# Kernel optimization log

Measured on AMD Instinct MI355X. Metric: run time of the kernel, lower is better.

Reference implementation:

```python
import jax, jax.numpy as jnp
import numpy as np
from jax import lax

B, T, S, D = 16, 16, 196, 768
H = 256          # hidden_dim
NH = 4           # attention heads
TH = 32          # temporal hidden = max(16, H//8)
UP = 4           # UPSAMPLE_FACTOR


def _ln(x, w, b):
    m = jnp.mean(x, -1, keepdims=True)
    v = jnp.mean((x - m) ** 2, -1, keepdims=True)
    return (x - m) / jnp.sqrt(v + 1e-5) * w + b


def _gelu(x):
    return jax.nn.gelu(x, approximate=False)  # torch nn.GELU default (erf)


def _upmat(g, f):
    # torch F.interpolate bilinear, align_corners=False, as a [g*f, g] matrix
    g_up = g * f
    src = np.maximum((np.arange(g_up) + 0.5) / f - 0.5, 0.0)
    i0 = np.minimum(np.floor(src).astype(np.int64), g - 1)
    i1 = np.minimum(i0 + 1, g - 1)
    w1 = (src - i0).astype(np.float32)
    w0 = 1.0 - w1
    W = np.zeros((g_up, g), dtype=np.float32)
    np.add.at(W, (np.arange(g_up), i0), w0)
    np.add.at(W, (np.arange(g_up), i1), w1)
    return jnp.asarray(W)


def setup_inputs() -> dict:
    key = jax.random.key(0)
    ks = jax.random.split(key, 12)
    r = lambda i, shape: jax.random.normal(ks[i], shape, jnp.float32) * 0.02
    return dict(
        tokens=jax.random.normal(ks[0], (B, T * S, D), jnp.float32),
        num_frames=T,
        fixed_box_wh=jax.random.uniform(ks[1], (2,), jnp.float32, 0.1, 0.5),
        ln_w=jnp.ones((D,), jnp.float32), ln_b=jnp.zeros((D,), jnp.float32),
        query=r(2, (1, 1, D)),
        in_proj_w=r(3, (3 * D, D)), in_proj_b=jnp.zeros((3 * D,), jnp.float32),
        out_w=r(4, (D, D)), out_b=jnp.zeros((D,), jnp.float32),
        an_w=jnp.ones((D,), jnp.float32), an_b=jnp.zeros((D,), jnp.float32),
        obj_w=r(5, (1, D)), obj_b=jnp.zeros((1,), jnp.float32),
        temperature=jnp.asarray(8.0, jnp.float32),
        r1_w=r(6, (H, 2 * D)), r1_b=jnp.zeros((H,), jnp.float32),
        r2_w=r(7, (H // 2, H)), r2_b=jnp.zeros((H // 2,), jnp.float32),
        r3_w=r(8, (2, H // 2)), r3_b=jnp.zeros((2,), jnp.float32),
        tc1_w=r(9, (TH, 2, 5)), tc1_b=jnp.zeros((TH,), jnp.float32),
        tc2_w=r(10, (2, TH, 5)), tc2_b=jnp.zeros((2,), jnp.float32),
    )


def reference(tokens, num_frames, fixed_box_wh, ln_w, ln_b, query,
              in_proj_w, in_proj_b, out_w, out_b, an_w, an_b, obj_w, obj_b,
              temperature, r1_w, r1_b, r2_w, r2_b, r3_w, r3_b,
              tc1_w, tc1_b, tc2_w, tc2_b):
    Bb, N, Dd = tokens.shape
    Tt = int(num_frames)
    Ss = N // Tt
    g = int(round(Ss ** 0.5))
    g_up = g * UP
    BT = Bb * Tt
    dt = tokens.dtype

    normed = _ln(tokens, ln_w, ln_b)
    flat = normed.reshape(BT, Ss, Dd)  # per-frame tokens

    # --- attention pooling with learned query (dropout off, eval) ---
    Wq, Wk, Wv = jnp.split(in_proj_w, 3, 0)
    bq, bk, bv = jnp.split(in_proj_b, 3, 0)
    dh = Dd // NH
    qh = (query.reshape(1, Dd) @ Wq.T + bq).reshape(NH, dh)  # same query for all frames
    kh = (flat @ Wk.T + bk).reshape(BT, Ss, NH, dh)
    vh = (flat @ Wv.T + bv).reshape(BT, Ss, NH, dh)
    scores = jnp.einsum('hd,bshd->bhs', qh, kh) / jnp.sqrt(jnp.asarray(dh, dt))
    attnp = jax.nn.softmax(scores, -1)
    ctx = jnp.einsum('bhs,bshd->bhd', attnp, vh).reshape(BT, Dd)
    pooled = _ln(ctx @ out_w.T + out_b, an_w, an_b)

    obj = (flat @ obj_w.T + obj_b)[..., 0]  # [BT,S]
    Wu = _upmat(g, UP)
    up = jnp.einsum('ug,bgh,vh->buv', Wu, obj.reshape(BT, g, g), Wu)
    up = up.reshape(BT, g_up * g_up)
    temp = jnp.maximum(temperature, 1.0)
    probs = jax.nn.softmax(up * temp, -1)
    coords = (jnp.arange(g_up, dtype=dt) + 0.5) / g_up
    yy, xx = jnp.meshgrid(coords, coords, indexing='ij')
    cx0 = probs @ xx.reshape(-1)
    cy0 = probs @ yy.reshape(-1)

    # --- 3x3 local token gather around coarse center ---
    cxg = jnp.clip(cx0 * g, 0, g - 1).astype(jnp.int32)
    cyg = jnp.clip(cy0 * g, 0, g - 1).astype(jnp.int32)
    off = jnp.array([-1, 0, 1], jnp.int32)
    gy = jnp.clip(cyg[:, None, None] + off[None, :, None], 0, g - 1)
    gx = jnp.clip(cxg[:, None, None] + off[None, None, :], 0, g - 1)
    idx = (gy * g + gx).reshape(BT, 9)
    local = jnp.take_along_axis(flat, idx[:, :, None], axis=1).mean(1)

    # --- refine MLP ---
    h1 = _gelu(jnp.concatenate([pooled, local], -1) @ r1_w.T + r1_b)
    h2 = _gelu(h1 @ r2_w.T + r2_b)
    delta = h2 @ r3_w.T + r3_b
    cx = jnp.clip(cx0 + 0.3 * jnp.tanh(delta[:, 0]), 0.0, 1.0)
    cy = jnp.clip(cy0 + 0.3 * jnp.tanh(delta[:, 1]), 0.0, 1.0)

    # --- temporal residual refiner over center trajectories ---
    seq = jnp.stack([cx, cy], 1).reshape(Bb, Tt, 2).transpose(0, 2, 1)  # [B,2,T]
    dn = ('NCH', 'OIH', 'NCH')
    t1 = _gelu(lax.conv_general_dilated(seq, tc1_w, (1,), [(2, 2)],
                                        dimension_numbers=dn) + tc1_b[None, :, None])
    td = lax.conv_general_dilated(t1, tc2_w, (1,), [(2, 2)],
                                  dimension_numbers=dn) + tc2_b[None, :, None]
    td = td.transpose(0, 2, 1).reshape(BT, 2)
    cx = jnp.clip(cx + 0.12 * jnp.tanh(td[:, 0]), 0.0, 1.0)
    cy = jnp.clip(cy + 0.12 * jnp.tanh(td[:, 1]), 0.0, 1.0)

    # --- fixed-size boxes ---
    min_size = 1.0 / g
    wh = jnp.clip(jnp.broadcast_to(fixed_box_wh.reshape(1, 2), (Bb, 2)), min_size, 1.0)
    wh = jnp.broadcast_to(wh[:, None, :], (Bb, Tt, 2)).reshape(BT, 2)
    w, h = wh[:, 0], wh[:, 1]
    x1 = jnp.clip(cx - 0.5 * w, 0.0, 1.0)
    y1 = jnp.clip(cy - 0.5 * h, 0.0, 1.0)
    x2 = jnp.clip(cx + 0.5 * w, 0.0, 1.0)
    y2 = jnp.clip(cy + 0.5 * h, 0.0, 1.0)
    x2 = jnp.clip(jnp.maximum(x2, x1 + min_size), 0.0, 1.0)
    y2 = jnp.clip(jnp.maximum(y2, y1 + min_size), 0.0, 1.0)
    return jnp.stack([x1, y1, x2, y2], 1).reshape(Bb, Tt, 4)
```

## Files before the change

### kernel.cpp

```cpp
#include <hip/hip_runtime.h>
#include <hip/hip_bf16.h>
#include <math.h>

#define SS 196
#define DD 768

__device__ __forceinline__ float b2f(ushort u){
  union { unsigned int i; float f; } v; v.i = ((unsigned int)u) << 16; return v.f;
}
__device__ __forceinline__ bool bfmode(const void* lnw){
  return ((const ushort*)lnw)[0] != 0;
}
__device__ __forceinline__ float ldx(const void* p, size_t i, bool bf){
  return bf ? b2f(((const ushort*)p)[i]) : ((const float*)p)[i];
}
__device__ __forceinline__ float gelu_f(float x){
  return 0.5f * x * (1.0f + erff(x * 0.70710678118654752f));
}
__device__ __forceinline__ float wredsum(float v){
  #pragma unroll
  for(int o=32;o;o>>=1) v += __shfl_xor(v,o,64);
  return v;
}
__device__ __forceinline__ float wredmax(float v){
  #pragma unroll
  for(int o=32;o;o>>=1) v = fmaxf(v, __shfl_xor(v,o,64));
  return v;
}

__global__ __launch_bounds__(256) void k_qh(const void* __restrict__ q,
                                            const void* __restrict__ wq,
                                            const void* __restrict__ bq,
                                            const void* __restrict__ flagp,
                                            float* __restrict__ qh){
  bool bf = bfmode(flagp);
  int wv = threadIdx.x >> 6, lane = threadIdx.x & 63;
  int c = blockIdx.x * 4 + wv;
  float acc = 0.f;
  #pragma unroll
  for(int i=0;i<12;i++){ int d = lane + 64*i; acc += ldx(q,d,bf) * ldx(wq,(size_t)c*DD+d,bf); }
  acc = wredsum(acc);
  if(lane==0) qh[c] = acc + ldx(bq,c,bf);
}

__global__ __launch_bounds__(256) void k_wkeff(const void* __restrict__ wproj,
                                               const float* __restrict__ qh,
                                               const void* __restrict__ lnw,
                                               const void* __restrict__ objw,
                                               float* __restrict__ wkraw,
                                               float* __restrict__ wf){
  bool bf = bfmode(lnw);
  int idx = blockIdx.x*256 + threadIdx.x;
  int h = idx / DD, d = idx - h*DD;
  size_t base = ((size_t)(DD + h*192))*DD + d;
  const float* qp = qh + h*192;
  float acc = 0.f;
  #pragma unroll 8
  for(int j=0;j<192;j++) acc += qp[j] * ldx(wproj, base + (size_t)j*DD, bf);
  wkraw[idx] = acc;
  float w = ldx(lnw,d,bf);
  wf[idx] = w * acc;
  if(h==0) wf[4*DD + d] = w * ldx(objw,d,bf);
}

__global__ __launch_bounds__(256) void k_consts(const float* __restrict__ wf,
                                                const float* __restrict__ wkraw,
                                                const void* __restrict__ lnb,
                                                const void* __restrict__ objw,
                                                const void* __restrict__ flagp,
                                                float* __restrict__ s12){
  bool bf = bfmode(flagp);
  int wv = threadIdx.x >> 6, lane = threadIdx.x & 63;
  for(int r = wv; r < 10; r += 4){
    float acc = 0.f;
    #pragma unroll
    for(int i=0;i<12;i++){
      int d = lane + 64*i;
      if(r < 5)      acc += wf[r*DD + d];
      else if(r < 9) acc += ldx(lnb,d,bf) * wkraw[(r-5)*DD + d];
      else           acc += ldx(lnb,d,bf) * ldx(objw,d,bf);
    }
    acc = wredsum(acc);
    if(lane==0) s12[r] = acc;
  }
}

__global__ __launch_bounds__(256) void k_pass1(const void* __restrict__ tok,
                                               const float* __restrict__ wf,
                                               const float* __restrict__ s12,
                                               const void* __restrict__ objb,
                                               const void* __restrict__ flagp,
                                               float* __restrict__ scores,
                                               float* __restrict__ objv,
                                               float* __restrict__ meanv,
                                               float* __restrict__ rstdv){
  __shared__ __align__(16) float swf[5*DD];
  __shared__ float ss12[10];
  for(int i=threadIdx.x;i<5*DD;i+=256) swf[i]=wf[i];
  if(threadIdx.x<10) ss12[threadIdx.x]=s12[threadIdx.x];
  __syncthreads();
  bool bf = bfmode(flagp);
  int wv = threadIdx.x >> 6, lane = threadIdx.x & 63;
  for(int it=0; it<4; it++){
    int tkn = blockIdx.x*16 + wv*4 + it;
    int f = tkn / SS, s = tkn - f*SS;
    float a0=0,a1=0,a2=0,a3=0,a4=0,sm=0,sq=0;
    if(bf){
      const ushort* x = (const ushort*)tok + (size_t)tkn * DD;
      #pragma unroll
      for(int i=0;i<3;i++){
        int d = 4*lane + 256*i;
        ushort4 u = *(const ushort4*)(x + d);
        float x0=b2f(u.x), x1=b2f(u.y), x2=b2f(u.z), x3=b2f(u.w);
        sm += (x0+x1)+(x2+x3); sq += (x0*x0+x1*x1)+(x2*x2+x3*x3);
        float4 w;
        w = *(const float4*)&swf[0*DD+d]; a0 += x0*w.x + x1*w.y + x2*w.z + x3*w.w;
        w = *(const float4*)&swf[1*DD+d]; a1 += x0*w.x + x1*w.y + x2*w.z + x3*w.w;
        w = *(const float4*)&swf[2*DD+d]; a2 += x0*w.x + x1*w.y + x2*w.z + x3*w.w;
        w = *(const float4*)&swf[3*DD+d]; a3 += x0*w.x + x1*w.y + x2*w.z + x3*w.w;
        w = *(const float4*)&swf[4*DD+d]; a4 += x0*w.x + x1*w.y + x2*w.z + x3*w.w;
      }
    } else {
      const float* x = (const float*)tok + (size_t)tkn * DD;
      #pragma unroll
      for(int i=0;i<3;i++){
        int d = 4*lane + 256*i;
        float4 u = *(const float4*)(x + d);
        sm += u.x+u.y+u.z+u.w;
        sq += u.x*u.x+u.y*u.y+u.z*u.z+u.w*u.w;
        float4 w;
        w = *(const float4*)&swf[0*DD+d]; a0 += u.x*w.x+u.y*w.y+u.z*w.z+u.w*w.w;
        w = *(const float4*)&swf[1*DD+d]; a1 += u.x*w.x+u.y*w.y+u.z*w.z+u.w*w.w;
        w = *(const float4*)&swf[2*DD+d]; a2 += u.x*w.x+u.y*w.y+u.z*w.z+u.w*w.w;
        w = *(const float4*)&swf[3*DD+d]; a3 += u.x*w.x+u.y*w.y+u.z*w.z+u.w*w.w;
        w = *(const float4*)&swf[4*DD+d]; a4 += u.x*w.x+u.y*w.y+u.z*w.z+u.w*w.w;
      }
    }
    sm=wredsum(sm); sq=wredsum(sq);
    a0=wredsum(a0); a1=wredsum(a1); a2=wredsum(a2); a3=wredsum(a3); a4=wredsum(a4);
    if(lane==0){
      const float invD = 1.0f/768.0f;
      float m = sm*invD;
      float var = sq*invD - m*m;
      float rstd = rsqrtf(var + 1e-5f);
      meanv[tkn]=m; rstdv[tkn]=rstd;
      const float sc = 0.07216878364870322f;
      scores[(f*4+0)*SS+s] = (rstd*(a0 - m*ss12[0]) + ss12[5]) * sc;
      scores[(f*4+1)*SS+s] = (rstd*(a1 - m*ss12[1]) + ss12[6]) * sc;
      scores[(f*4+2)*SS+s] = (rstd*(a2 - m*ss12[2]) + ss12[7]) * sc;
      scores[(f*4+3)*SS+s] = (rstd*(a3 - m*ss12[3]) + ss12[8]) * sc;
      objv[tkn] = rstd*(a4 - m*ss12[4]) + ss12[9] + ldx(objb,0,bf);
    }
  }
}

__global__ __launch_bounds__(256) void k_soft(const float* __restrict__ rstdv,
                                              const float* __restrict__ meanv,
                                              float* __restrict__ scores,
                                              float* __restrict__ cterm){
  int f = blockIdx.x;
  int h = threadIdx.x >> 6, lane = threadIdx.x & 63;
  float* sc = scores + (size_t)(f*4+h)*SS;
  const float* rs = rstdv + f*SS;
  const float* mv = meanv + f*SS;
  float v[4]; float mx = -1e30f;
  #pragma unroll
  for(int j=0;j<4;j++){ int s=lane+64*j; v[j] = (s<SS)? sc[s] : -1e30f; mx=fmaxf(mx,v[j]); }
  mx = wredmax(mx);
  float e[4], sum=0.f;
  #pragma unroll
  for(int j=0;j<4;j++){ int s=lane+64*j; e[j] = (s<SS)? expf(v[j]-mx) : 0.f; sum += e[j]; }
  sum = wredsum(sum);
  float inv = 1.0f/sum;
  float cp = 0.f;
  #pragma unroll
  for(int j=0;j<4;j++){
    int s=lane+64*j;
    if(s<SS){ float r=rs[s]; float a=e[j]*inv*r; sc[s]=a; cp += a*mv[s]; }
  }
  cp = wredsum(cp);
  if(lane==0) cterm[f*4+h] = cp;
}

__global__ __launch_bounds__(256) void k_xbar(const void* __restrict__ tok,
                                              const float* __restrict__ aw,
                                              const float* __restrict__ cterm,
                                              const void* __restrict__ lnw,
                                              const void* __restrict__ lnb,
                                              float* __restrict__ xbar){
  bool bf = bfmode(lnw);
  int f = blockIdx.x;
  __shared__ float a4[SS*4];
  for(int i=threadIdx.x;i<SS*4;i+=256){ int s=i>>2, h=i&3; a4[i]=aw[(size_t)(f*4+h)*SS+s]; }
  __syncthreads();
  float acc[3][4] = {};
  if(bf){
    const ushort* tf = (const ushort*)tok + (size_t)f*SS*DD;
    for(int s=0;s<SS;s++){
      float w0=a4[s*4+0], w1=a4[s*4+1], w2=a4[s*4+2], w3=a4[s*4+3];
      #pragma unroll
      for(int j=0;j<3;j++){
        float x = b2f(tf[(size_t)s*DD + threadIdx.x + 256*j]);
        acc[j][0]+=w0*x; acc[j][1]+=w1*x; acc[j][2]+=w2*x; acc[j][3]+=w3*x;
      }
    }
  } else {
    const float* tf = (const float*)tok + (size_t)f*SS*DD;
    for(int s=0;s<SS;s++){
      float w0=a4[s*4+0], w1=a4[s*4+1], w2=a4[s*4+2], w3=a4[s*4+3];
      #pragma unroll
      for(int j=0;j<3;j++){
        float x = tf[(size_t)s*DD + threadIdx.x + 256*j];
        acc[j][0]+=w0*x; acc[j][1]+=w1*x; acc[j][2]+=w2*x; acc[j][3]+=w3*x;
      }
    }
  }
  float c0=cterm[f*4+0], c1=cterm[f*4+1], c2=cterm[f*4+2], c3=cterm[f*4+3];
  #pragma unroll
  for(int j=0;j<3;j++){
    int d = threadIdx.x + 256*j;
    float w=ldx(lnw,d,bf), b=ldx(lnb,d,bf);
    xbar[((size_t)(f*4+0))*DD+d] = w*(acc[j][0]-c0)+b;
    xbar[((size_t)(f*4+1))*DD+d] = w*(acc[j][1]-c1)+b;
    xbar[((size_t)(f*4+2))*DD+d] = w*(acc[j][2]-c2)+b;
    xbar[((size_t)(f*4+3))*DD+d] = w*(acc[j][3]-c3)+b;
  }
}

template<int N, int K, int ACT, int CTX, int ROWOFF>
__global__ __launch_bounds__(256) void k_tgemm(const float* __restrict__ A,
                                               const void* __restrict__ W,
                                               const void* __restrict__ bias,
                                               const void* __restrict__ flagp,
                                               float* __restrict__ C){
  bool bf = bfmode(flagp);
  __shared__ float As[32][32];
  __shared__ float Bs[32][64];
  int tid = threadIdx.x;
  int n0 = blockIdx.x*64, m0 = blockIdx.y*32;
  int h  = n0 / 192;
  int am = tid>>3, ak = (tid&7)*4;
  int bn = tid>>2, bk = (tid&3)*8;
  const float* ap = A + (CTX ? ((size_t)((m0+am)*4+h))*768 : (size_t)(m0+am)*K) + ak;
  const ushort* wpb = (const ushort*)W + (size_t)(ROWOFF+n0+bn)*K + bk;
  const float*  wpf = (const float*)W  + (size_t)(ROWOFF+n0+bn)*K + bk;
  int tx = tid&15, ty = tid>>4;
  float acc[2][4] = {};
  float4 av; float b8[8];
  av = *(const float4*)ap;
  if(bf){
    ushort4 w0 = *(const ushort4*)(wpb);
    ushort4 w1 = *(const ushort4*)(wpb+4);
    b8[0]=b2f(w0.x); b8[1]=b2f(w0.y); b8[2]=b2f(w0.z); b8[3]=b2f(w0.w);
    b8[4]=b2f(w1.x); b8[5]=b2f(w1.y); b8[6]=b2f(w1.z); b8[7]=b2f(w1.w);
  } else {
    float4 w0 = *(const float4*)(wpf);
    float4 w1 = *(const float4*)(wpf+4);
    b8[0]=w0.x; b8[1]=w0.y; b8[2]=w0.z; b8[3]=w0.w;
// ... 36 lines not shown
        bv2=ldx(bias,ROWOFF+n+2,bf), bv3=ldx(bias,ROWOFF+n+3,bf);
  #pragma unroll
  for(int i=0;i<2;i++){
    int m = m0 + ty*2 + i;
    float4 o;
    o.x=acc[i][0]+bv0; o.y=acc[i][1]+bv1; o.z=acc[i][2]+bv2; o.w=acc[i][3]+bv3;
    if(ACT){ o.x=gelu_f(o.x); o.y=gelu_f(o.y); o.z=gelu_f(o.z); o.w=gelu_f(o.w); }
    *(float4*)&C[(size_t)m*N + n] = o;
  }
}

__global__ __launch_bounds__(256) void k_lnan(const float* __restrict__ X,
                                              const void* __restrict__ anw,
                                              const void* __restrict__ anb,
                                              const void* __restrict__ flagp,
                                              float* __restrict__ pl){
  bool bf = bfmode(flagp);
  int wv = threadIdx.x >> 6, lane = threadIdx.x & 63;
  int f = blockIdx.x*4 + wv;
  const float* x = X + (size_t)f*DD;
  float v[12]; float sm=0, sq=0;
  #pragma unroll
  for(int i=0;i<12;i++){ v[i]=x[lane+64*i]; sm+=v[i]; sq+=v[i]*v[i]; }
  sm=wredsum(sm); sq=wredsum(sq);
  float m = sm*(1.0f/768.0f);
  float rstd = rsqrtf(sq*(1.0f/768.0f) - m*m + 1e-5f);
  #pragma unroll
  for(int i=0;i<12;i++){
    int d = lane+64*i;
    pl[(size_t)f*1536 + d] = (v[i]-m)*rstd*ldx(anw,d,bf) + ldx(anb,d,bf);
  }
}

__global__ __launch_bounds__(256) void k_obj(const void* __restrict__ tok,
                                             const float* __restrict__ objv,
                                             const float* __restrict__ meanv,
                                             const float* __restrict__ rstdv,
                                             const void* __restrict__ temp,
                                             const void* __restrict__ lnw,
                                             const void* __restrict__ lnb,
                                             float* __restrict__ pl,
                                             float* __restrict__ cxy){
  bool bf = bfmode(lnw);
  int f = blockIdx.x;
  int tid = threadIdx.x;
  __shared__ float G[196];
  __shared__ float up[3136];
  __shared__ int   i0a[56], i1a[56];
  __shared__ float w0a[56], w1a[56];
  __shared__ float redm[4], reds[4], redx[4], redy[4];
  __shared__ int   sidx[9];
  __shared__ float rj[9], rmj[9];
  if(tid<196) G[tid] = objv[(size_t)f*SS + tid];
  if(tid<56){
    float src = fmaxf((tid+0.5f)*0.25f - 0.5f, 0.0f);
    int i0 = min((int)floorf(src), 13);
    i0a[tid]=i0; i1a[tid]=min(i0+1,13);
    float w1 = src - (float)i0;
    w1a[tid]=w1; w0a[tid]=1.0f-w1;
  }
  __syncthreads();
  float lmax = -1e30f;
  for(int i=tid;i<3136;i+=256){
    int u=i/56, v=i-u*56;
    float val = w0a[u]*(w0a[v]*G[i0a[u]*14+i0a[v]] + w1a[v]*G[i0a[u]*14+i1a[v]])
              + w1a[u]*(w0a[v]*G[i1a[u]*14+i0a[v]] + w1a[v]*G[i1a[u]*14+i1a[v]]);
    up[i]=val; lmax=fmaxf(lmax,val);
  }
  lmax = wredmax(lmax);
  if((tid&63)==0) redm[tid>>6]=lmax;
  __syncthreads();
  float mx = fmaxf(fmaxf(redm[0],redm[1]), fmaxf(redm[2],redm[3]));
  float t = fmaxf(ldx(temp,0,bf), 1.0f);
  float se=0, sx=0, sy=0;
  for(int i=tid;i<3136;i+=256){
    int u=i/56, v=i-u*56;
    float e = expf((up[i]-mx)*t);
    se += e;
    sx += e * ((v+0.5f)*(1.0f/56.0f));
    sy += e * ((u+0.5f)*(1.0f/56.0f));
  }
  se=wredsum(se); sx=wredsum(sx); sy=wredsum(sy);
  if((tid&63)==0){ reds[tid>>6]=se; redx[tid>>6]=sx; redy[tid>>6]=sy; }
  __syncthreads();
  se = reds[0]+reds[1]+reds[2]+reds[3];
  sx = redx[0]+redx[1]+redx[2]+redx[3];
  sy = redy[0]+redy[1]+redy[2]+redy[3];
  float cx0 = sx/se, cy0 = sy/se;
  if(tid==0){ cxy[f*2]=cx0; cxy[f*2+1]=cy0; }
  float vx = fminf(fmaxf(cx0*14.0f,0.0f),13.0f); int cxg=(int)vx;
  float vy = fminf(fmaxf(cy0*14.0f,0.0f),13.0f); int cyg=(int)vy;
  if(tid<9){
    int dy = tid/3 - 1, dx = tid%3 - 1;
    int gy = min(max(cyg+dy,0),13), gx = min(max(cxg+dx,0),13);
    int s = gy*14+gx;
    sidx[tid]=s;
    float r = rstdv[(size_t)f*SS+s];
    rj[tid]=r; rmj[tid]=r*meanv[(size_t)f*SS+s];
  }
  __syncthreads();
  float offc = 0.f;
  #pragma unroll
  for(int j=0;j<9;j++) offc += rmj[j];
  for(int d=tid; d<DD; d+=256){
    float acc = 0.f;
    #pragma unroll
    for(int j=0;j<9;j++) acc += rj[j]*ldx(tok, (size_t)f*SS*DD + (size_t)sidx[j]*DD + d, bf);
    pl[(size_t)f*1536 + DD + d] = ldx(lnw,d,bf)*((acc-offc)*(1.0f/9.0f)) + ldx(lnb,d,bf);
  }
}

__global__ __launch_bounds__(256) void k_final(const float* __restrict__ h2,
                                               const void* __restrict__ r3w,
                                               const void* __restrict__ r3b,
                                               const float* __restrict__ cxy,
                                               const void* __restrict__ tc1w,
                                               const void* __restrict__ tc1b,
                                               const void* __restrict__ tc2w,
                                               const void* __restrict__ tc2b,
                                               const void* __restrict__ fbw,
                                               const void* __restrict__ flagp,
                                               void* __restrict__ out){
  bool bf = bfmode(flagp);
  __shared__ float sxs[256], sys[256];
  __shared__ float t1[16*32*16];
  __shared__ float td[16*2*16];
  int f = threadIdx.x;
  float a0=0.f, a1=0.f;
  const float* hh = h2 + (size_t)f*128;
  for(int k=0;k<128;k++){ float x=hh[k]; a0 += x*ldx(r3w,k,bf); a1 += x*ldx(r3w,128+k,bf); }
  a0 += ldx(r3b,0,bf); a1 += ldx(r3b,1,bf);
  float cx1 = fminf(fmaxf(cxy[f*2]   + 0.3f*tanhf(a0), 0.f), 1.f);
  float cy1 = fminf(fmaxf(cxy[f*2+1] + 0.3f*tanhf(a1), 0.f), 1.f);
  sxs[f]=cx1; sys[f]=cy1;
  __syncthreads();
  for(int idx=f; idx<8192; idx+=256){
    int b = idx>>9, o = (idx>>4)&31, t = idx&15;
    float acc = ldx(tc1b,o,bf);
    #pragma unroll
    for(int k=0;k<5;k++){
      int tt = t + k - 2;
      if(tt>=0 && tt<16)
        acc += sxs[b*16+tt]*ldx(tc1w,o*10 + k,bf) + sys[b*16+tt]*ldx(tc1w,o*10 + 5 + k,bf);
    }
// ... 44 lines not shown
                              void* d_out, int out_size, void* d_ws, size_t ws_size,
                              hipStream_t stream){
  (void)in_sizes; (void)n_in; (void)out_size; (void)ws_size;
  const void* tok   = d_in[0];
  const void* fbw   = d_in[2];
  const void* lnw   = d_in[3];
  const void* lnb   = d_in[4];
  const void* query = d_in[5];
  const void* wproj = d_in[6];
  const void* bproj = d_in[7];
  const void* outw  = d_in[8];
  const void* outb  = d_in[9];
  const void* anw   = d_in[10];
  const void* anb   = d_in[11];
  const void* objw  = d_in[12];
  const void* objb  = d_in[13];
  const void* temp  = d_in[14];
  const void* r1w   = d_in[15];
  const void* r1b   = d_in[16];
  const void* r2w   = d_in[17];
  const void* r2b   = d_in[18];
  const void* r3w   = d_in[19];
  const void* r3b   = d_in[20];
  const void* tc1w  = d_in[21];
  const void* tc1b  = d_in[22];
  const void* tc2w  = d_in[23];
  const void* tc2b  = d_in[24];

  float* ws    = (float*)d_ws;
  float* qh    = ws;
  float* wkraw = ws + 768;
  float* wf    = wkraw + 3072;
  float* s12   = wf + 3840;
  float* scores= s12 + 16;
  float* objv  = scores + 200704;
  float* meanv = objv + 50176;
  float* rstdv = meanv + 50176;
  float* cterm = rstdv + 50176;
  float* xbar  = cterm + 1024;
  float* ctx   = xbar + 786432;
  float* ppre  = ctx + 196608;
  float* pl    = ppre + 196608;
  float* h1    = pl + 393216;
  float* h2    = h1 + 65536;
  float* cxy   = h2 + 32768;

  hipLaunchKernelGGL(k_qh,    dim3(192),  dim3(256), 0, stream, query, wproj, bproj, lnw, qh);
  hipLaunchKernelGGL(k_wkeff, dim3(12),   dim3(256), 0, stream, wproj, qh, lnw, objw, wkraw, wf);
  hipLaunchKernelGGL(k_consts,dim3(1),    dim3(256), 0, stream, wf, wkraw, lnb, objw, lnw, s12);
  hipLaunchKernelGGL(k_pass1, dim3(3136), dim3(256), 0, stream, tok, wf, s12, objb, lnw, scores, objv, meanv, rstdv);
  hipLaunchKernelGGL(k_soft,  dim3(256),  dim3(256), 0, stream, rstdv, meanv, scores, cterm);
  hipLaunchKernelGGL(k_xbar,  dim3(256),  dim3(256), 0, stream, tok, scores, cterm, lnw, lnb, xbar);
  hipLaunchKernelGGL((k_tgemm<768,768,0,1,1536>), dim3(12,8), dim3(256), 0, stream, xbar, wproj, bproj, lnw, ctx);
  hipLaunchKernelGGL((k_tgemm<768,768,0,0,0>),    dim3(12,8), dim3(256), 0, stream, ctx, outw, outb, lnw, ppre);
  hipLaunchKernelGGL(k_lnan,  dim3(64),   dim3(256), 0, stream, ppre, anw, anb, lnw, pl);
  hipLaunchKernelGGL(k_obj,   dim3(256),  dim3(256), 0, stream, tok, objv, meanv, rstdv, temp, lnw, lnb, pl, cxy);
  hipLaunchKernelGGL((k_tgemm<256,1536,1,0,0>), dim3(4,8), dim3(256), 0, stream, pl, r1w, r1b, lnw, h1);
  hipLaunchKernelGGL((k_tgemm<128,256,1,0,0>),  dim3(2,8), dim3(256), 0, stream, h1, r2w, r2b, lnw, h2);
  hipLaunchKernelGGL(k_final, dim3(1),    dim3(256), 0, stream, h2, r3w, r3b, cxy, tc1w, tc1b, tc2w, tc2b, fbw, lnw, (void*)d_out);
}
```

Measured before the change: 539.1 us.

## Split xbar reduction across token chunks and fold q-projection into wkeff

The attention-weighted token sum now runs as 256x4 blocks over 49-token chunks, with partials written to a workspace and summed by a separate combine kernel. This raises parallelism over a kernel that previously used only 256 blocks to stream all token data. The q projection kernel is removed; each wkeff block recomputes its head's 192 q values into shared memory before the key-weight contraction. The cost is one more launch, extra partial traffic, and redundant q work inside wkeff.

```diff
diff --git a/kernel.cpp b/kernel.cpp
--- a/kernel.cpp
+++ b/kernel.cpp
@@ -28,35 +28,34 @@
   return v;
 }
 
-__global__ __launch_bounds__(256) void k_qh(const void* __restrict__ q,
-                                            const void* __restrict__ wq,
-                                            const void* __restrict__ bq,
-                                            const void* __restrict__ flagp,
-                                            float* __restrict__ qh){
-  bool bf = bfmode(flagp);
-  int wv = threadIdx.x >> 6, lane = threadIdx.x & 63;
-  int c = blockIdx.x * 4 + wv;
-  float acc = 0.f;
-  #pragma unroll
-  for(int i=0;i<12;i++){ int d = lane + 64*i; acc += ldx(q,d,bf) * ldx(wq,(size_t)c*DD+d,bf); }
-  acc = wredsum(acc);
-  if(lane==0) qh[c] = acc + ldx(bq,c,bf);
-}
-
 __global__ __launch_bounds__(256) void k_wkeff(const void* __restrict__ wproj,
-                                               const float* __restrict__ qh,
+                                               const void* __restrict__ query,
+                                               const void* __restrict__ bproj,
                                                const void* __restrict__ lnw,
                                                const void* __restrict__ objw,
                                                float* __restrict__ wkraw,
                                                float* __restrict__ wf){
   bool bf = bfmode(lnw);
+  __shared__ float sq[DD];
+  __shared__ float sqh[192];
   int idx = blockIdx.x*256 + threadIdx.x;
   int h = idx / DD, d = idx - h*DD;
+  for(int i=threadIdx.x;i<DD;i+=256) sq[i]=ldx(query,i,bf);
+  __syncthreads();
+  int wv = threadIdx.x >> 6, lane = threadIdx.x & 63;
+  for(int j=wv; j<192; j+=4){
+    size_t row = (size_t)(h*192 + j)*DD;
+    float acc = 0.f;
+    #pragma unroll
+    for(int i=0;i<12;i++){ int dd = lane + 64*i; acc += sq[dd]*ldx(wproj, row+dd, bf); }
+    acc = wredsum(acc);
+    if(lane==0) sqh[j] = acc + ldx(bproj, h*192+j, bf);
+  }
+  __syncthreads();
   size_t base = ((size_t)(DD + h*192))*DD + d;
-  const float* qp = qh + h*192;
   float acc = 0.f;
   #pragma unroll 8
-  for(int j=0;j<192;j++) acc += qp[j] * ldx(wproj, base + (size_t)j*DD, bf);
+  for(int j=0;j<192;j++) acc += sqh[j] * ldx(wproj, base + (size_t)j*DD, bf);
   wkraw[idx] = acc;
   float w = ldx(lnw,d,bf);
   wf[idx] = w * acc;
@@ -182,21 +181,23 @@
   if(lane==0) cterm[f*4+h] = cp;
 }
 
-__global__ __launch_bounds__(256) void k_xbar(const void* __restrict__ tok,
-                                              const float* __restrict__ aw,
-                                              const float* __restrict__ cterm,
-                                              const void* __restrict__ lnw,
-                                              const void* __restrict__ lnb,
-                                              float* __restrict__ xbar){
-  bool bf = bfmode(lnw);
-  int f = blockIdx.x;
-  __shared__ float a4[SS*4];
-  for(int i=threadIdx.x;i<SS*4;i+=256){ int s=i>>2, h=i&3; a4[i]=aw[(size_t)(f*4+h)*SS+s]; }
+__global__ __launch_bounds__(256) void k_xbar_part(const void* __restrict__ tok,
+                                                   const float* __restrict__ aw,
+                                                   const void* __restrict__ flagp,
+                                                   float* __restrict__ xpart){
+  bool bf = bfmode(flagp);
+  int f = blockIdx.x, c = blockIdx.y;
+  __shared__ float a4[49*4];
+  for(int i=threadIdx.x;i<49*4;i+=256){
+    int s=i>>2, h=i&3;
+    a4[i]=aw[(size_t)(f*4+h)*SS + c*49 + s];
+  }
   __syncthreads();
   float acc[3][4] = {};
   if(bf){
-    const ushort* tf = (const ushort*)tok + (size_t)f*SS*DD;
-    for(int s=0;s<SS;s++){
+    const ushort* tf = (const ushort*)tok + (size_t)(f*SS + c*49)*DD;
+    #pragma unroll 7
+    for(int s=0;s<49;s++){
       float w0=a4[s*4+0], w1=a4[s*4+1], w2=a4[s*4+2], w3=a4[s*4+3];
       #pragma unroll
       for(int j=0;j<3;j++){
@@ -205,8 +206,9 @@
       }
     }
   } else {
-    const float* tf = (const float*)tok + (size_t)f*SS*DD;
-    for(int s=0;s<SS;s++){
+    const float* tf = (const float*)tok + (size_t)(f*SS + c*49)*DD;
+    #pragma unroll 7
+    for(int s=0;s<49;s++){
       float w0=a4[s*4+0], w1=a4[s*4+1], w2=a4[s*4+2], w3=a4[s*4+3];
       #pragma unroll
       for(int j=0;j<3;j++){
@@ -215,15 +217,42 @@
       }
     }
   }
+  #pragma unroll
+  for(int j=0;j<3;j++){
+    int d = threadIdx.x + 256*j;
+    size_t base = (((size_t)c*256 + f)*4)*DD + d;
+    xpart[base + 0*DD] = acc[j][0];
+    xpart[base + 1*DD] = acc[j][1];
+    xpart[base + 2*DD] = acc[j][2];
+    xpart[base + 3*DD] = acc[j][3];
+  }
+}
+
+__global__ __launch_bounds__(256) void k_xbar_comb(const float* __restrict__ xpart,
+                                                   const float* __restrict__ cterm,
+                                                   const void* __restrict__ lnw,
+                                                   const void* __restrict__ lnb,
+                                                   float* __restrict__ xbar){
+  bool bf = bfmode(lnw);
+  int f = blockIdx.x;
   float c0=cterm[f*4+0], c1=cterm[f*4+1], c2=cterm[f*4+2], c3=cterm[f*4+3];
   #pragma unroll
   for(int j=0;j<3;j++){
     int d = threadIdx.x + 256*j;
     float w=ldx(lnw,d,bf), b=ldx(lnb,d,bf);
-    xbar[((size_t)(f*4+0))*DD+d] = w*(acc[j][0]-c0)+b;
-    xbar[((size_t)(f*4+1))*DD+d] = w*(acc[j][1]-c1)+b;
-    xbar[((size_t)(f*4+2))*DD+d] = w*(acc[j][2]-c2)+b;
-    xbar[((size_t)(f*4+3))*DD+d] = w*(acc[j][3]-c3)+b;
+    float s0=0,s1=0,s2=0,s3=0;
+    #pragma unroll
+    for(int c=0;c<4;c++){
+      size_t base = (((size_t)c*256 + f)*4)*DD + d;
+      s0 += xpart[base + 0*DD];
+      s1 += xpart[base + 1*DD];
+      s2 += xpart[base + 2*DD];
+      s3 += xpart[base + 3*DD];
+    }
+    xbar[((size_t)(f*4+0))*DD+d] = w*(s0-c0)+b;
+    xbar[((size_t)(f*4+1))*DD+d] = w*(s1-c1)+b;
+    xbar[((size_t)(f*4+2))*DD+d] = w*(s2-c2)+b;
+    xbar[((size_t)(f*4+3))*DD+d] = w*(s3-c3)+b;
   }
 }
 
@@ -526,13 +555,15 @@
   float* h1    = pl + 393216;
   float* h2    = h1 + 65536;
   float* cxy   = h2 + 32768;
-
-  hipLaunchKernelGGL(k_qh,    dim3(192),  dim3(256), 0, stream, query, wproj, bproj, lnw, qh);
-  hipLaunchKernelGGL(k_wkeff, dim3(12),   dim3(256), 0, stream, wproj, qh, lnw, objw, wkraw, wf);
+  float* xpart = cxy + 512;
+  (void)qh;
+
+  hipLaunchKernelGGL(k_wkeff, dim3(12),   dim3(256), 0, stream, wproj, query, bproj, lnw, objw, wkraw, wf);
   hipLaunchKernelGGL(k_consts,dim3(1),    dim3(256), 0, stream, wf, wkraw, lnb, objw, lnw, s12);
   hipLaunchKernelGGL(k_pass1, dim3(3136), dim3(256), 0, stream, tok, wf, s12, objb, lnw, scores, objv, meanv, rstdv);
   hipLaunchKernelGGL(k_soft,  dim3(256),  dim3(256), 0, stream, rstdv, meanv, scores, cterm);
-  hipLaunchKernelGGL(k_xbar,  dim3(256),  dim3(256), 0, stream, tok, scores, cterm, lnw, lnb, xbar);
+  hipLaunchKernelGGL(k_xbar_part, dim3(256,4), dim3(256), 0, stream, tok, scores, lnw, xpart);
+  hipLaunchKernelGGL(k_xbar_comb, dim3(256),   dim3(256), 0, stream, xpart, cterm, lnw, lnb, xbar);
   hipLaunchKernelGGL((k_tgemm<768,768,0,1,1536>), dim3(12,8), dim3(256), 0, stream, xbar, wproj, bproj, lnw, ctx);
   hipLaunchKernelGGL((k_tgemm<768,768,0,0,0>),    dim3(12,8), dim3(256), 0, stream, ctx, outw, outb, lnw, ppre);
   hipLaunchKernelGGL(k_lnan,  dim3(64),   dim3(256), 0, stream, ppre, anw, anb, lnw, pl);
```

New measurement: 590.6 us. 9.6% more time.

## Fuse per-frame LN stats, softmax, xbar and objectness into one kernel; split wkeff reduction

Applied to the files above, without the earlier changes.

Merges pass1, softmax, xbar pooling and the objectness/upsample/centroid kernel into a single per-frame kernel of 512 threads. Scores, means, rstd and objectness now stay in shared memory instead of going through global scratch, and the frame's tokens are read while they may still be in cache. The wkeff reduction is split over 16 partial chunks with a combine kernel to get more parallelism. The cost is only 256 blocks for the main token pass instead of 3136, which may leave less memory-level parallelism, plus heavier shared memory use per block.

```diff
diff --git a/kernel.cpp b/kernel.cpp
--- a/kernel.cpp
+++ b/kernel.cpp
@@ -43,23 +43,36 @@
   if(lane==0) qh[c] = acc + ldx(bq,c,bf);
 }
 
-__global__ __launch_bounds__(256) void k_wkeff(const void* __restrict__ wproj,
-                                               const float* __restrict__ qh,
-                                               const void* __restrict__ lnw,
-                                               const void* __restrict__ objw,
-                                               float* __restrict__ wkraw,
-                                               float* __restrict__ wf){
+__global__ __launch_bounds__(256) void k_wkpart(const void* __restrict__ wproj,
+                                                const float* __restrict__ qh,
+                                                const void* __restrict__ flagp,
+                                                float* __restrict__ wkp){
+  bool bf = bfmode(flagp);
+  int idx = blockIdx.x*256 + threadIdx.x;
+  int h = idx / DD, d = idx - h*DD;
+  int c = blockIdx.y;
+  const float* qp = qh + h*192 + c*12;
+  size_t base = ((size_t)(DD + h*192 + c*12))*DD + d;
+  float acc = 0.f;
+  #pragma unroll
+  for(int j=0;j<12;j++) acc += qp[j] * ldx(wproj, base + (size_t)j*DD, bf);
+  wkp[(size_t)c*3072 + idx] = acc;
+}
+
+__global__ __launch_bounds__(256) void k_wkcomb(const float* __restrict__ wkp,
+                                                const void* __restrict__ lnw,
+                                                const void* __restrict__ objw,
+                                                float* __restrict__ wkraw,
+                                                float* __restrict__ wf){
   bool bf = bfmode(lnw);
   int idx = blockIdx.x*256 + threadIdx.x;
   int h = idx / DD, d = idx - h*DD;
-  size_t base = ((size_t)(DD + h*192))*DD + d;
-  const float* qp = qh + h*192;
-  float acc = 0.f;
-  #pragma unroll 8
-  for(int j=0;j<192;j++) acc += qp[j] * ldx(wproj, base + (size_t)j*DD, bf);
-  wkraw[idx] = acc;
+  float s = 0.f;
+  #pragma unroll
+  for(int c=0;c<16;c++) s += wkp[(size_t)c*3072 + idx];
+  wkraw[idx] = s;
   float w = ldx(lnw,d,bf);
-  wf[idx] = w * acc;
+  wf[idx] = w * s;
   if(h==0) wf[4*DD + d] = w * ldx(objw,d,bf);
 }
 
@@ -85,33 +98,65 @@
   }
 }
 
-__global__ __launch_bounds__(256) void k_pass1(const void* __restrict__ tok,
+__global__ __launch_bounds__(512) void k_frame(const void* __restrict__ tok,
                                                const float* __restrict__ wf,
                                                const float* __restrict__ s12,
                                                const void* __restrict__ objb,
-                                               const void* __restrict__ flagp,
-                                               float* __restrict__ scores,
-                                               float* __restrict__ objv,
-                                               float* __restrict__ meanv,
-                                               float* __restrict__ rstdv){
+                                               const void* __restrict__ temp,
+                                               const void* __restrict__ lnw,
+                                               const void* __restrict__ lnb,
+                                               float* __restrict__ xbar,
+                                               float* __restrict__ pl,
+                                               float* __restrict__ cxy){
+  bool bf = bfmode(lnw);
   __shared__ __align__(16) float swf[5*DD];
   __shared__ float ss12[10];
-  for(int i=threadIdx.x;i<5*DD;i+=256) swf[i]=wf[i];
-  if(threadIdx.x<10) ss12[threadIdx.x]=s12[threadIdx.x];
-  __syncthreads();
-  bool bf = bfmode(flagp);
-  int wv = threadIdx.x >> 6, lane = threadIdx.x & 63;
-  for(int it=0; it<4; it++){
-    int tkn = blockIdx.x*16 + wv*4 + it;
-    int f = tkn / SS, s = tkn - f*SS;
-    float a0=0,a1=0,a2=0,a3=0,a4=0,sm=0,sq=0;
-    if(bf){
-      const ushort* x = (const ushort*)tok + (size_t)tkn * DD;
+  __shared__ float ssc[4][SS];
+  __shared__ float smean[SS], srstd[SS], sobj[SS];
+  __shared__ float sa4[SS*4];
+  __shared__ float scterm[4];
+  __shared__ float up[3136];
+  __shared__ int   i0a[56], i1a[56];
+  __shared__ float w0a[56], w1a[56];
+  __shared__ float redm[4], reds[8], redx[8], redy[8];
+  __shared__ int   sidx[9];
+  __shared__ float rj[9], rmj[9];
+  int tid = threadIdx.x;
+  int f = blockIdx.x;
+  int wv = tid >> 6, lane = tid & 63;
+  for(int i=tid;i<5*DD;i+=512) swf[i]=wf[i];
+  if(tid<10) ss12[tid]=s12[tid];
+  if(tid<56){
+    float src = fmaxf((tid+0.5f)*0.25f - 0.5f, 0.0f);
+    int i0 = min((int)floorf(src), 13);
+    i0a[tid]=i0; i1a[tid]=min(i0+1,13);
+    float w1 = src - (float)i0;
+    w1a[tid]=w1; w0a[tid]=1.0f-w1;
+  }
+  __syncthreads();
+  float objb0 = ldx(objb,0,bf);
+  const float sc = 0.07216878364870322f;
+  if(bf){
+    const ushort* xb = (const ushort*)tok + (size_t)f*SS*DD + 4*lane;
+    int s = wv;
+    ushort4 c0={0,0,0,0},c1={0,0,0,0},c2={0,0,0,0};
+    if(s<SS){
+      const ushort* x = xb + (size_t)s*DD;
+      c0=*(const ushort4*)(x); c1=*(const ushort4*)(x+256); c2=*(const ushort4*)(x+512);
+    }
+    while(s<SS){
+      int sn = s+8;
+      ushort4 n0=c0,n1=c1,n2=c2;
+      if(sn<SS){
+        const ushort* x = xb + (size_t)sn*DD;
+        n0=*(const ushort4*)(x); n1=*(const ushort4*)(x+256); n2=*(const ushort4*)(x+512);
+      }
+      float a0=0,a1=0,a2=0,a3=0,a4=0,sm=0,sq=0;
+      ushort4 uu[3] = {c0,c1,c2};
       #pragma unroll
       for(int i=0;i<3;i++){
         int d = 4*lane + 256*i;
-        ushort4 u = *(const ushort4*)(x + d);
-        float x0=b2f(u.x), x1=b2f(u.y), x2=b2f(u.z), x3=b2f(u.w);
+        float x0=b2f(uu[i].x), x1=b2f(uu[i].y), x2=b2f(uu[i].z), x3=b2f(uu[i].w);
         sm += (x0+x1)+(x2+x3); sq += (x0*x0+x1*x1)+(x2*x2+x3*x3);
         float4 w;
         w = *(const float4*)&swf[0*DD+d]; a0 += x0*w.x + x1*w.y + x2*w.z + x3*w.w;
@@ -120,14 +165,44 @@
         w = *(const float4*)&swf[3*DD+d]; a3 += x0*w.x + x1*w.y + x2*w.z + x3*w.w;
         w = *(const float4*)&swf[4*DD+d]; a4 += x0*w.x + x1*w.y + x2*w.z + x3*w.w;
       }
-    } else {
-      const float* x = (const float*)tok + (size_t)tkn * DD;
+      sm=wredsum(sm); sq=wredsum(sq);
+      a0=wredsum(a0); a1=wredsum(a1); a2=wredsum(a2); a3=wredsum(a3); a4=wredsum(a4);
+      if(lane==0){
+        const float invD = 1.0f/768.0f;
+        float m = sm*invD;
+        float var = sq*invD - m*m;
+        float rstd = rsqrtf(var + 1e-5f);
+        smean[s]=m; srstd[s]=rstd;
+        ssc[0][s] = (rstd*(a0 - m*ss12[0]) + ss12[5]) * sc;
+        ssc[1][s] = (rstd*(a1 - m*ss12[1]) + ss12[6]) * sc;
+        ssc[2][s] = (rstd*(a2 - m*ss12[2]) + ss12[7]) * sc;
+        ssc[3][s] = (rstd*(a3 - m*ss12[3]) + ss12[8]) * sc;
+        sobj[s] = rstd*(a4 - m*ss12[4]) + ss12[9] + objb0;
+      }
+      s = sn; c0=n0; c1=n1; c2=n2;
+    }
+  } else {
+    const float* xb = (const float*)tok + (size_t)f*SS*DD + 4*lane;
+    int s = wv;
+    float4 c0={0,0,0,0},c1={0,0,0,0},c2={0,0,0,0};
+    if(s<SS){
+      const float* x = xb + (size_t)s*DD;
+      c0=*(const float4*)(x); c1=*(const float4*)(x+256); c2=*(const float4*)(x+512);
+    }
+    while(s<SS){
+      int sn = s+8;
+      float4 n0=c0,n1=c1,n2=c2;
+      if(sn<SS){
+        const float* x = xb + (size_t)sn*DD;
+        n0=*(const float4*)(x); n1=*(const float4*)(x+256); n2=*(const float4*)(x+512);
+      }
+      float a0=0,a1=0,a2=0,a3=0,a4=0,sm=0,sq=0;
+      float4 uu[3] = {c0,c1,c2};
       #pragma unroll
       for(int i=0;i<3;i++){
         int d = 4*lane + 256*i;
-        float4 u = *(const float4*)(x + d);
-        sm += u.x+u.y+u.z+u.w;
-        sq += u.x*u.x+u.y*u.y+u.z*u.z+u.w*u.w;
+        float4 u = uu[i];
+        sm += (u.x+u.y)+(u.z+u.w); sq += (u.x*u.x+u.y*u.y)+(u.z*u.z+u.w*u.w);
         float4 w;
         w = *(const float4*)&swf[0*DD+d]; a0 += u.x*w.x+u.y*w.y+u.z*w.z+u.w*w.w;
         w = *(const float4*)&swf[1*DD+d]; a1 += u.x*w.x+u.y*w.y+u.z*w.z+u.w*w.w;
@@ -135,95 +210,138 @@
         w = *(const float4*)&swf[3*DD+d]; a3 += u.x*w.x+u.y*w.y+u.z*w.z+u.w*w.w;
         w = *(const float4*)&swf[4*DD+d]; a4 += u.x*w.x+u.y*w.y+u.z*w.z+u.w*w.w;
       }
-    }
-    sm=wredsum(sm); sq=wredsum(sq);
-    a0=wredsum(a0); a1=wredsum(a1); a2=wredsum(a2); a3=wredsum(a3); a4=wredsum(a4);
-    if(lane==0){
-      const float invD = 1.0f/768.0f;
-      float m = sm*invD;
-      float var = sq*invD - m*m;
-      float rstd = rsqrtf(var + 1e-5f);
-      meanv[tkn]=m; rstdv[tkn]=rstd;
-      const float sc = 0.07216878364870322f;
-      scores[(f*4+0)*SS+s] = (rstd*(a0 - m*ss12[0]) + ss12[5]) * sc;
-      scores[(f*4+1)*SS+s] = (rstd*(a1 - m*ss12[1]) + ss12[6]) * sc;
-      scores[(f*4+2)*SS+s] = (rstd*(a2 - m*ss12[2]) + ss12[7]) * sc;
-      scores[(f*4+3)*SS+s] = (rstd*(a3 - m*ss12[3]) + ss12[8]) * sc;
-      objv[tkn] = rstd*(a4 - m*ss12[4]) + ss12[9] + ldx(objb,0,bf);
-    }
-  }
-}
-
-__global__ __launch_bounds__(256) void k_soft(const float* __restrict__ rstdv,
-                                              const float* __restrict__ meanv,
-                                              float* __restrict__ scores,
-                                              float* __restrict__ cterm){
-  int f = blockIdx.x;
-  int h = threadIdx.x >> 6, lane = threadIdx.x & 63;
-  float* sc = scores + (size_t)(f*4+h)*SS;
-  const float* rs = rstdv + f*SS;
-  const float* mv = meanv + f*SS;
-  float v[4]; float mx = -1e30f;
-  #pragma unroll
-  for(int j=0;j<4;j++){ int s=lane+64*j; v[j] = (s<SS)? sc[s] : -1e30f; mx=fmaxf(mx,v[j]); }
-  mx = wredmax(mx);
-  float e[4], sum=0.f;
-  #pragma unroll
-  for(int j=0;j<4;j++){ int s=lane+64*j; e[j] = (s<SS)? expf(v[j]-mx) : 0.f; sum += e[j]; }
-  sum = wredsum(sum);
-  float inv = 1.0f/sum;
-  float cp = 0.f;
-  #pragma unroll
-  for(int j=0;j<4;j++){
-    int s=lane+64*j;
-    if(s<SS){ float r=rs[s]; float a=e[j]*inv*r; sc[s]=a; cp += a*mv[s]; }
-  }
-  cp = wredsum(cp);
-  if(lane==0) cterm[f*4+h] = cp;
-}
-
-__global__ __launch_bounds__(256) void k_xbar(const void* __restrict__ tok,
-                                              const float* __restrict__ aw,
-                                              const float* __restrict__ cterm,
-                                              const void* __restrict__ lnw,
-                                              const void* __restrict__ lnb,
-                                              float* __restrict__ xbar){
-  bool bf = bfmode(lnw);
-  int f = blockIdx.x;
-  __shared__ float a4[SS*4];
-  for(int i=threadIdx.x;i<SS*4;i+=256){ int s=i>>2, h=i&3; a4[i]=aw[(size_t)(f*4+h)*SS+s]; }
-  __syncthreads();
-  float acc[3][4] = {};
-  if(bf){
-    const ushort* tf = (const ushort*)tok + (size_t)f*SS*DD;
-    for(int s=0;s<SS;s++){
-      float w0=a4[s*4+0], w1=a4[s*4+1], w2=a4[s*4+2], w3=a4[s*4+3];
-      #pragma unroll
-      for(int j=0;j<3;j++){
-        float x = b2f(tf[(size_t)s*DD + threadIdx.x + 256*j]);
-        acc[j][0]+=w0*x; acc[j][1]+=w1*x; acc[j][2]+=w2*x; acc[j][3]+=w3*x;
-      }
-    }
+      sm=wredsum(sm); sq=wredsum(sq);
+      a0=wredsum(a0); a1=wredsum(a1); a2=wredsum(a2); a3=wredsum(a3); a4=wredsum(a4);
+      if(lane==0){
+        const float invD = 1.0f/768.0f;
+        float m = sm*invD;
+        float var = sq*invD - m*m;
+        float rstd = rsqrtf(var + 1e-5f);
+        smean[s]=m; srstd[s]=rstd;
+        ssc[0][s] = (rstd*(a0 - m*ss12[0]) + ss12[5]) * sc;
+        ssc[1][s] = (rstd*(a1 - m*ss12[1]) + ss12[6]) * sc;
+        ssc[2][s] = (rstd*(a2 - m*ss12[2]) + ss12[7]) * sc;
+        ssc[3][s] = (rstd*(a3 - m*ss12[3]) + ss12[8]) * sc;
+        sobj[s] = rstd*(a4 - m*ss12[4]) + ss12[9] + objb0;
+      }
+      s = sn; c0=n0; c1=n1; c2=n2;
+    }
+  }
+  __syncthreads();
+  if(wv < 4){
+    int h = wv;
+    float v[4]; float mx = -1e30f;
+    #pragma unroll
+    for(int j=0;j<4;j++){ int s=lane+64*j; v[j] = (s<SS)? ssc[h][s] : -1e30f; mx=fmaxf(mx,v[j]); }
+    mx = wredmax(mx);
+    float e[4], sum=0.f;
+    #pragma unroll
+    for(int j=0;j<4;j++){ int s=lane+64*j; e[j] = (s<SS)? expf(v[j]-mx) : 0.f; sum += e[j]; }
+    sum = wredsum(sum);
+    float inv = 1.0f/sum;
+    float cp = 0.f;
+    #pragma unroll
+    for(int j=0;j<4;j++){
+      int s=lane+64*j;
+      if(s<SS){ float r=srstd[s]; float a=e[j]*inv*r; sa4[s*4+h]=a; cp += a*smean[s]; }
+    }
+    cp = wredsum(cp);
+    if(lane==0) scterm[h] = cp;
   } else {
-    const float* tf = (const float*)tok + (size_t)f*SS*DD;
-    for(int s=0;s<SS;s++){
-      float w0=a4[s*4+0], w1=a4[s*4+1], w2=a4[s*4+2], w3=a4[s*4+3];
-      #pragma unroll
-      for(int j=0;j<3;j++){
-        float x = tf[(size_t)s*DD + threadIdx.x + 256*j];
-        acc[j][0]+=w0*x; acc[j][1]+=w1*x; acc[j][2]+=w2*x; acc[j][3]+=w3*x;
-      }
-    }
-  }
-  float c0=cterm[f*4+0], c1=cterm[f*4+1], c2=cterm[f*4+2], c3=cterm[f*4+3];
-  #pragma unroll
-  for(int j=0;j<3;j++){
-    int d = threadIdx.x + 256*j;
-    float w=ldx(lnw,d,bf), b=ldx(lnb,d,bf);
-    xbar[((size_t)(f*4+0))*DD+d] = w*(acc[j][0]-c0)+b;
-    xbar[((size_t)(f*4+1))*DD+d] = w*(acc[j][1]-c1)+b;
-    xbar[((size_t)(f*4+2))*DD+d] = w*(acc[j][2]-c2)+b;
-    xbar[((size_t)(f*4+3))*DD+d] = w*(acc[j][3]-c3)+b;
+    int w4 = wv-4;
+    float lmax = -1e30f;
+    for(int i = w4*64 + lane; i<3136; i+=256){
+      int u=i/56, v=i-u*56;
+      float val = w0a[u]*(w0a[v]*sobj[i0a[u]*14+i0a[v]] + w1a[v]*sobj[i0a[u]*14+i1a[v]])
+                + w1a[u]*(w0a[v]*sobj[i1a[u]*14+i0a[v]] + w1a[v]*sobj[i1a[u]*14+i1a[v]]);
+      up[i]=val; lmax=fmaxf(lmax,val);
+    }
+    lmax = wredmax(lmax);
+    if(lane==0) redm[w4]=lmax;
+  }
+  __syncthreads();
+  float mx = fmaxf(fmaxf(redm[0],redm[1]), fmaxf(redm[2],redm[3]));
+  float t = fmaxf(ldx(temp,0,bf), 1.0f);
+  float se=0, sx=0, sy=0;
+  for(int i=tid;i<3136;i+=512){
+    int u=i/56, v=i-u*56;
+    float e = expf((up[i]-mx)*t);
+    se += e;
+    sx += e * ((v+0.5f)*(1.0f/56.0f));
+    sy += e * ((u+0.5f)*(1.0f/56.0f));
+  }
+  se=wredsum(se); sx=wredsum(sx); sy=wredsum(sy);
+  if(lane==0){ reds[wv]=se; redx[wv]=sx; redy[wv]=sy; }
+  __syncthreads();
+  se=0; sx=0; sy=0;
+  #pragma unroll
+  for(int i=0;i<8;i++){ se+=reds[i]; sx+=redx[i]; sy+=redy[i]; }
+  float cx0 = sx/se, cy0 = sy/se;
+  if(tid==0){ cxy[f*2]=cx0; cxy[f*2+1]=cy0; }
+  float vx = fminf(fmaxf(cx0*14.0f,0.0f),13.0f); int cxg=(int)vx;
+  float vy = fminf(fmaxf(cy0*14.0f,0.0f),13.0f); int cyg=(int)vy;
+  if(tid<9){
+    int dy = tid/3 - 1, dx = tid%3 - 1;
+    int gy = min(max(cyg+dy,0),13), gx = min(max(cxg+dx,0),13);
+    int s = gy*14+gx;
+    sidx[tid]=s;
+    float r = srstd[s];
+    rj[tid]=r; rmj[tid]=r*smean[s];
+  }
+  __syncthreads();
+  float c0=scterm[0], c1=scterm[1], c2=scterm[2], c3=scterm[3];
+  {
+    float A0=0,A1=0,A2=0,A3=0,B0=0,B1=0,B2=0,B3=0;
+    if(bf){
+      const ushort* tf = (const ushort*)tok + (size_t)f*SS*DD;
+      #pragma unroll 4
+      for(int s=0;s<SS;s++){
+        float w0=sa4[s*4+0], w1=sa4[s*4+1], w2=sa4[s*4+2], w3=sa4[s*4+3];
+        float x0 = b2f(tf[(size_t)s*DD + tid]);
+        A0+=w0*x0; A1+=w1*x0; A2+=w2*x0; A3+=w3*x0;
+        if(tid<256){
+          float x1 = b2f(tf[(size_t)s*DD + tid + 512]);
+          B0+=w0*x1; B1+=w1*x1; B2+=w2*x1; B3+=w3*x1;
+        }
+      }
+    } else {
+      const float* tf = (const float*)tok + (size_t)f*SS*DD;
+      #pragma unroll 4
+      for(int s=0;s<SS;s++){
+        float w0=sa4[s*4+0], w1=sa4[s*4+1], w2=sa4[s*4+2], w3=sa4[s*4+3];
+        float x0 = tf[(size_t)s*DD + tid];
+        A0+=w0*x0; A1+=w1*x0; A2+=w2*x0; A3+=w3*x0;
+        if(tid<256){
+          float x1 = tf[(size_t)s*DD + tid + 512];
+          B0+=w0*x1; B1+=w1*x1; B2+=w2*x1; B3+=w3*x1;
+        }
+      }
+    }
+    {
+      int d = tid;
+      float w=ldx(lnw,d,bf), b=ldx(lnb,d,bf);
+      xbar[((size_t)(f*4+0))*DD+d] = w*(A0-c0)+b;
+      xbar[((size_t)(f*4+1))*DD+d] = w*(A1-c1)+b;
+      xbar[((size_t)(f*4+2))*DD+d] = w*(A2-c2)+b;
+      xbar[((size_t)(f*4+3))*DD+d] = w*(A3-c3)+b;
+    }
+    if(tid<256){
+      int d = tid + 512;
+      float w=ldx(lnw,d,bf), b=ldx(lnb,d,bf);
+      xbar[((size_t)(f*4+0))*DD+d] = w*(B0-c0)+b;
+      xbar[((size_t)(f*4+1))*DD+d] = w*(B1-c1)+b;
+      xbar[((size_t)(f*4+2))*DD+d] = w*(B2-c2)+b;
+      xbar[((size_t)(f*4+3))*DD+d] = w*(B3-c3)+b;
+    }
+  }
+  float offc = 0.f;
+  #pragma unroll
+  for(int j=0;j<9;j++) offc += rmj[j];
+  for(int d=tid; d<DD; d+=512){
+    float acc = 0.f;
+    #pragma unroll
+    for(int j=0;j<9;j++) acc += rj[j]*ldx(tok, (size_t)f*SS*DD + (size_t)sidx[j]*DD + d, bf);
+    pl[(size_t)f*1536 + DD + d] = ldx(lnw,d,bf)*((acc-offc)*(1.0f/9.0f)) + ldx(lnb,d,bf);
   }
 }
 
@@ -326,84 +444,6 @@
   }
 }
 
-__global__ __launch_bounds__(256) void k_obj(const void* __restrict__ tok,
-                                             const float* __restrict__ objv,
-                                             const float* __restrict__ meanv,
-                                             const float* __restrict__ rstdv,
-                                             const void* __restrict__ temp,
-                                             const void* __restrict__ lnw,
-                                             const void* __restrict__ lnb,
-                                             float* __restrict__ pl,
-                                             float* __restrict__ cxy){
-  bool bf = bfmode(lnw);
-  int f = blockIdx.x;
-  int tid = threadIdx.x;
-  __shared__ float G[196];
-  __shared__ float up[3136];
-  __shared__ int   i0a[56], i1a[56];
-  __shared__ float w0a[56], w1a[56];
-  __shared__ float redm[4], reds[4], redx[4], redy[4];
-  __shared__ int   sidx[9];
-  __shared__ float rj[9], rmj[9];
-  if(tid<196) G[tid] = objv[(size_t)f*SS + tid];
-  if(tid<56){
-    float src = fmaxf((tid+0.5f)*0.25f - 0.5f, 0.0f);
-    int i0 = min((int)floorf(src), 13);
-    i0a[tid]=i0; i1a[tid]=min(i0+1,13);
-    float w1 = src - (float)i0;
-    w1a[tid]=w1; w0a[tid]=1.0f-w1;
-  }
-  __syncthreads();
-  float lmax = -1e30f;
-  for(int i=tid;i<3136;i+=256){
-    int u=i/56, v=i-u*56;
-    float val = w0a[u]*(w0a[v]*G[i0a[u]*14+i0a[v]] + w1a[v]*G[i0a[u]*14+i1a[v]])
-              + w1a[u]*(w0a[v]*G[i1a[u]*14+i0a[v]] + w1a[v]*G[i1a[u]*14+i1a[v]]);
-    up[i]=val; lmax=fmaxf(lmax,val);
-  }
-  lmax = wredmax(lmax);
-  if((tid&63)==0) redm[tid>>6]=lmax;
-  __syncthreads();
-  float mx = fmaxf(fmaxf(redm[0],redm[1]), fmaxf(redm[2],redm[3]));
-  float t = fmaxf(ldx(temp,0,bf), 1.0f);
-  float se=0, sx=0, sy=0;
-  for(int i=tid;i<3136;i+=256){
-    int u=i/56, v=i-u*56;
-    float e = expf((up[i]-mx)*t);
-    se += e;
-    sx += e * ((v+0.5f)*(1.0f/56.0f));
-    sy += e * ((u+0.5f)*(1.0f/56.0f));
-  }
-  se=wredsum(se); sx=wredsum(sx); sy=wredsum(sy);
-  if((tid&63)==0){ reds[tid>>6]=se; redx[tid>>6]=sx; redy[tid>>6]=sy; }
-  __syncthreads();
-  se = reds[0]+reds[1]+reds[2]+reds[3];
-  sx = redx[0]+redx[1]+redx[2]+redx[3];
-  sy = redy[0]+redy[1]+redy[2]+redy[3];
-  float cx0 = sx/se, cy0 = sy/se;
-  if(tid==0){ cxy[f*2]=cx0; cxy[f*2+1]=cy0; }
-  float vx = fminf(fmaxf(cx0*14.0f,0.0f),13.0f); int cxg=(int)vx;
-  float vy = fminf(fmaxf(cy0*14.0f,0.0f),13.0f); int cyg=(int)vy;
-  if(tid<9){
-    int dy = tid/3 - 1, dx = tid%3 - 1;
-    int gy = min(max(cyg+dy,0),13), gx = min(max(cxg+dx,0),13);
-    int s = gy*14+gx;
-    sidx[tid]=s;
-    float r = rstdv[(size_t)f*SS+s];
-    rj[tid]=r; rmj[tid]=r*meanv[(size_t)f*SS+s];
-  }
-  __syncthreads();
-  float offc = 0.f;
-  #pragma unroll
-  for(int j=0;j<9;j++) offc += rmj[j];
-  for(int d=tid; d<DD; d+=256){
-    float acc = 0.f;
-    #pragma unroll
-    for(int j=0;j<9;j++) acc += rj[j]*ldx(tok, (size_t)f*SS*DD + (size_t)sidx[j]*DD + d, bf);
-    pl[(size_t)f*1536 + DD + d] = ldx(lnw,d,bf)*((acc-offc)*(1.0f/9.0f)) + ldx(lnb,d,bf);
-  }
-}
-
 __global__ __launch_bounds__(256) void k_final(const float* __restrict__ h2,
                                                const void* __restrict__ r3w,
                                                const void* __restrict__ r3b,
@@ -514,12 +554,8 @@
   float* wkraw = ws + 768;
   float* wf    = wkraw + 3072;
   float* s12   = wf + 3840;
-  float* scores= s12 + 16;
-  float* objv  = scores + 200704;
-  float* meanv = objv + 50176;
-  float* rstdv = meanv + 50176;
-  float* cterm = rstdv + 50176;
-  float* xbar  = cterm + 1024;
+  float* wkp   = s12 + 16;
+  float* xbar  = wkp + 49152;
   float* ctx   = xbar + 786432;
   float* ppre  = ctx + 196608;
   float* pl    = ppre + 196608;
@@ -527,17 +563,15 @@
   float* h2    = h1 + 65536;
   float* cxy   = h2 + 32768;
 
-  hipLaunchKernelGGL(k_qh,    dim3(192),  dim3(256), 0, stream, query, wproj, bproj, lnw, qh);
-  hipLaunchKernelGGL(k_wkeff, dim3(12),   dim3(256), 0, stream, wproj, qh, lnw, objw, wkraw, wf);
-  hipLaunchKernelGGL(k_consts,dim3(1),    dim3(256), 0, stream, wf, wkraw, lnb, objw, lnw, s12);
-  hipLaunchKernelGGL(k_pass1, dim3(3136), dim3(256), 0, stream, tok, wf, s12, objb, lnw, scores, objv, meanv, rstdv);
-  hipLaunchKernelGGL(k_soft,  dim3(256),  dim3(256), 0, stream, rstdv, meanv, scores, cterm);
-  hipLaunchKernelGGL(k_xbar,  dim3(256),  dim3(256), 0, stream, tok, scores, cterm, lnw, lnb, xbar);
+  hipLaunchKernelGGL(k_qh,     dim3(192),    dim3(256), 0, stream, query, wproj, bproj, lnw, qh);
+  hipLaunchKernelGGL(k_wkpart, dim3(12,16),  dim3(256), 0, stream, wproj, qh, lnw, wkp);
+  hipLaunchKernelGGL(k_wkcomb, dim3(12),     dim3(256), 0, stream, wkp, lnw, objw, wkraw, wf);
+  hipLaunchKernelGGL(k_consts, dim3(1),      dim3(256), 0, stream, wf, wkraw, lnb, objw, lnw, s12);
+  hipLaunchKernelGGL(k_frame,  dim3(256),    dim3(512), 0, stream, tok, wf, s12, objb, temp, lnw, lnb, xbar, pl, cxy);
   hipLaunchKernelGGL((k_tgemm<768,768,0,1,1536>), dim3(12,8), dim3(256), 0, stream, xbar, wproj, bproj, lnw, ctx);
   hipLaunchKernelGGL((k_tgemm<768,768,0,0,0>),    dim3(12,8), dim3(256), 0, stream, ctx, outw, outb, lnw, ppre);
-  hipLaunchKernelGGL(k_lnan,  dim3(64),   dim3(256), 0, stream, ppre, anw, anb, lnw, pl);
-  hipLaunchKernelGGL(k_obj,   dim3(256),  dim3(256), 0, stream, tok, objv, meanv, rstdv, temp, lnw, lnb, pl, cxy);
+  hipLaunchKernelGGL(k_lnan,   dim3(64),     dim3(256), 0, stream, ppre, anw, anb, lnw, pl);
   hipLaunchKernelGGL((k_tgemm<256,1536,1,0,0>), dim3(4,8), dim3(256), 0, stream, pl, r1w, r1b, lnw, h1);
   hipLaunchKernelGGL((k_tgemm<128,256,1,0,0>),  dim3(2,8), dim3(256), 0, stream, h1, r2w, r2b, lnw, h2);
-  hipLaunchKernelGGL(k_final, dim3(1),    dim3(256), 0, stream, h2, r3w, r3b, cxy, tc1w, tc1b, tc2w, tc2b, fbw, lnw, (void*)d_out);
-}
+  hipLaunchKernelGGL(k_final,  dim3(1),      dim3(256), 0, stream, h2, r3w, r3b, cxy, tc1w, tc1b, tc2w, tc2b, fbw, lnw, (void*)d_out);
+}
```

After: 536.3 us. No clear change (-0.5%).
